# Kernel optimization log

Measured on AMD Instinct MI355X. Metric: run time of the kernel, lower is better.

The kernel has to match this reference:

```python
import jax, jax.numpy as jnp
import numpy as np

B, S, D, H, E = 4, 1024, 1024, 4096, 8


def setup_inputs() -> dict:
    key = jax.random.key(0)
    ks = jax.random.split(key, 5)
    sd = 1.0 / np.sqrt(D)
    sh = 1.0 / np.sqrt(H)
    x = jax.random.normal(ks[0], (B, S, D), dtype=jnp.float32)
    # stacked expert weights: Linear(D->H), ReLU, Linear(H->D)
    W1 = jax.random.normal(ks[1], (E, D, H), dtype=jnp.float32) * sd
    b1 = jnp.zeros((E, H), dtype=jnp.float32)
    W2 = jax.random.normal(ks[2], (E, H, D), dtype=jnp.float32) * sh
    b2 = jnp.zeros((E, D), dtype=jnp.float32)
    # gate Linear(D->E)
    Wg = jax.random.normal(ks[3], (D, E), dtype=jnp.float32) * sd
    bg = jnp.zeros((E,), dtype=jnp.float32)
    return {"x": x, "W1": W1, "b1": b1, "W2": W2, "b2": b2,
            "Wg": Wg, "bg": bg, "top_k": 2}


def reference(x, W1, b1, W2, b2, Wg, bg, top_k):
    # gating
    gating_scores = jnp.einsum('bsd,de->bse', x, Wg) + bg          # [B,S,E]
    gating_probs = jax.nn.softmax(gating_scores, axis=-1)
    _, top_k_indices = jax.lax.top_k(gating_probs, top_k)          # [B,S,K]
    n_exp = Wg.shape[1]
    # per-token 0/1 mask of selected experts (matches torch sum over k of mask)
    # NOTE: original code multiplies by the binary mask only; top_k_probs are
    # computed but NOT used as combine weights. We reproduce that faithfully.
    sel = jnp.sum(top_k_indices[..., None] == jnp.arange(n_exp), axis=2)  # [B,S,E]
    sel = sel.astype(x.dtype)
    # dense all-experts FFN (as the original does)
    h = jax.nn.relu(jnp.einsum('bsd,edh->bseh', x, W1) + b1)       # [B,S,E,H]
    eo = jnp.einsum('bseh,ehd->bsed', h, W2) + b2                  # [B,S,E,D]
    output = jnp.einsum('bsed,bse->bsd', eo, sel)                  # [B,S,D]
    return (output, gating_scores)
```

## Files before the change

kernel.cpp:

```cpp
#include <hip/hip_runtime.h>
#include <hip/hip_bf16.h>
#include <stdint.h>

#define B_ 4
#define S_ 1024
#define D_ 1024
#define H_ 4096
#define E_ 8
#define T_ (B_*S_)

#define BM 256
#define BN 256
#define BK 64

typedef __bf16 bf16x8 __attribute__((ext_vector_type(8)));
typedef float f32x4 __attribute__((ext_vector_type(4)));
typedef unsigned short ushort8 __attribute__((ext_vector_type(8)));

__device__ __forceinline__ unsigned short f2bf(float f) {
  union { float f; uint32_t u; } v; v.f = f;
  uint32_t u = v.u;
  u += 0x7fff + ((u >> 16) & 1);
  return (unsigned short)(u >> 16);
}

__device__ __forceinline__ void gl16(const void* g, void* l) {
  __builtin_amdgcn_global_load_lds(
      (const __attribute__((address_space(1))) void*)g,
      (__attribute__((address_space(3))) void*)l,
      16, 0, 0);
}
#define MEMFENCE asm volatile("" ::: "memory")

__global__ __launch_bounds__(256) void conv_x_kernel(
    const float* __restrict__ x, unsigned short* __restrict__ xb) {
  size_t i = ((size_t)blockIdx.x * 256 + threadIdx.x) * 8;
  const float4* s = (const float4*)(x + i);
  float4 v0 = s[0], v1 = s[1];
  ushort8 w;
  w[0]=f2bf(v0.x); w[1]=f2bf(v0.y); w[2]=f2bf(v0.z); w[3]=f2bf(v0.w);
  w[4]=f2bf(v1.x); w[5]=f2bf(v1.y); w[6]=f2bf(v1.z); w[7]=f2bf(v1.w);
  *(ushort8*)(xb + i) = w;
}

__global__ __launch_bounds__(256) void transpose_conv(
    const float* __restrict__ in, unsigned short* __restrict__ outp,
    int R, int C) {
  __shared__ float tile[64][68];
  const int e = blockIdx.z;
  const size_t eoff = (size_t)e * R * C;
  const int r0 = blockIdx.y * 64, c0 = blockIdx.x * 64;
  const int t = threadIdx.x;
  {
    const int r = t >> 2, cq = (t & 3) * 16;
    const float4* s4 = (const float4*)(in + eoff + (size_t)(r0 + r) * C + (c0 + cq));
#pragma unroll
    for (int i = 0; i < 4; ++i)
      *(float4*)&tile[r][cq + i * 4] = s4[i];
  }
  __syncthreads();
  {
    const int c = t >> 2, r8 = (t & 3) * 16;
    unsigned short* dst = outp + eoff + (size_t)(c0 + c) * R + (r0 + r8);
    ushort8 w0, w1;
#pragma unroll
    for (int j = 0; j < 8; ++j) {
      w0[j] = f2bf(tile[r8 + j][c]);
      w1[j] = f2bf(tile[r8 + 8 + j][c]);
    }
    *(ushort8*)dst = w0;
    *(ushort8*)(dst + 8) = w1;
  }
}

__global__ __launch_bounds__(256) void gating_kernel(
    const float* __restrict__ x, const float* __restrict__ Wg,
    const float* __restrict__ bg, float* __restrict__ scores,
    int* __restrict__ cnt, int* __restrict__ lists) {
  int t = blockIdx.x * 4 + (threadIdx.x >> 6);
  int l = threadIdx.x & 63;
  float acc[E_];
#pragma unroll
  for (int e = 0; e < E_; ++e) acc[e] = 0.f;
  const float* xr = x + (size_t)t * D_;
  for (int k = l; k < D_; k += 64) {
    float xv = xr[k];
    const float4* w = (const float4*)(Wg + (size_t)k * E_);
    float4 w0 = w[0], w1 = w[1];
    acc[0] += xv * w0.x; acc[1] += xv * w0.y; acc[2] += xv * w0.z; acc[3] += xv * w0.w;
    acc[4] += xv * w1.x; acc[5] += xv * w1.y; acc[6] += xv * w1.z; acc[7] += xv * w1.w;
  }
#pragma unroll
  for (int off = 32; off > 0; off >>= 1)
#pragma unroll
    for (int e = 0; e < E_; ++e) acc[e] += __shfl_xor(acc[e], off, 64);
  if (l == 0) {
    float s[E_];
#pragma unroll
    for (int e = 0; e < E_; ++e) {
      s[e] = acc[e] + bg[e];
      scores[(size_t)t * E_ + e] = s[e];
    }
    int i1 = 0; float m1 = -1e30f;
#pragma unroll
    for (int e = 0; e < E_; ++e) if (s[e] > m1) { m1 = s[e]; i1 = e; }
    int i2 = -1; float m2 = -1e30f;
#pragma unroll
    for (int e = 0; e < E_; ++e) if (e != i1 && s[e] > m2) { m2 = s[e]; i2 = e; }
    int p1 = atomicAdd(&cnt[i1], 1); lists[i1 * T_ + p1] = t;
    int p2 = atomicAdd(&cnt[i2], 1); lists[i2 * T_ + p2] = t;
  }
}

__global__ void scan_kernel(const int* __restrict__ cnt, int* __restrict__ off) {
  if (threadIdx.x == 0) {
    int o = 0;
    for (int e = 0; e < E_; ++e) { off[e] = o; o += cnt[e]; }
  }
}

template <int LAYER, int SPLITK>
__global__ __launch_bounds__(512, 2) void ffn_gemm(
    const unsigned short* __restrict__ xb,
    const unsigned short* __restrict__ hbuf,
    const unsigned short* __restrict__ WT,
    const float* __restrict__ bias,
    const int* __restrict__ cnt, const int* __restrict__ off,
    const int* __restrict__ lists,
    unsigned short* __restrict__ hout,
    float* __restrict__ out)
{
  constexpr int K = (LAYER == 1) ? D_ : H_;
  constexpr int N = (LAYER == 1) ? H_ : D_;
  constexpr int KS = K / SPLITK;
  constexpr int NT = KS / BK;

  const int e    = blockIdx.z;
  const int nt_  = blockIdx.x % (N / BN);
  const int sp   = blockIdx.x / (N / BN);
  const int n0   = nt_ * BN;
  const int m0   = blockIdx.y * BM;
  const int k0   = sp * KS;
  const int count = cnt[e];
  if (m0 >= count) return;
  const int oe = off[e];
  const int* lst = lists + e * T_;

  __shared__ unsigned short sA[2][BM * BK];
  __shared__ unsigned short sB[2][BN * BK];

  const int tid  = threadIdx.x;
  const int lane = tid & 63;
  const int wv   = tid >> 6;
  const int wm   = (wv >> 2) * 128;
  const int wn   = (wv & 3) * 64;

  const int srow   = lane >> 3;
  const int schunk = (lane & 7) * 16;
  const int sgoff  = schunk ^ (srow << 4);

  const char* arow[4];
  const char* brow[4];
#pragma unroll
  for (int i = 0; i < 4; ++i) {
    int r  = i * 64 + wv * 8 + srow;
    int gr = m0 + r;
    if (LAYER == 1) {
      int tok = (gr < count) ? lst[gr] : lst[m0];
      arow[i] = (const char*)(xb + (size_t)tok * K + k0);
    } else {
      int rr = (gr < count) ? gr : m0;
      arow[i] = (const char*)(hbuf + (size_t)(oe + rr) * K + k0);
    }
    brow[i] = (const char*)(WT + (size_t)e * N * K + (size_t)(n0 + r) * K + k0);
  }

  auto stage = [&](int buf, int t) {
    const int kb = t * 128;
#pragma unroll
    for (int i = 0; i < 4; ++i)
      gl16(arow[i] + kb + sgoff, (char*)&sA[buf][0] + (i * 64 + wv * 8) * 128);
#pragma unroll
    for (int i = 0; i < 4; ++i)
      gl16(brow[i] + kb + sgoff, (char*)&sB[buf][0] + (i * 64 + wv * 8) * 128);
  };

  const int lrow = lane & 15;
  const int kg   = lane >> 4;
  const int fswz = (lrow & 7) << 4;

  f32x4 acc[8][4];
#pragma unroll
  for (int i = 0; i < 8; ++i)
#pragma unroll
    for (int j = 0; j < 4; ++j) acc[i][j] = (f32x4){0.f, 0.f, 0.f, 0.f};

  stage(0, 0);
  stage(1, 1);
  asm volatile("s_waitcnt vmcnt(8)" ::: "memory");
  __builtin_amdgcn_s_barrier();
  MEMFENCE;

  for (int t = 0; t < NT; ++t) {
    const int buf = t & 1;
    bf16x8 af[8][2], bfm[4][2];
#pragma unroll
    for (int i = 0; i < 8; ++i) {
      const int ra = wm + i * 16 + lrow;
#pragma unroll
      for (int ks = 0; ks < 2; ++ks)
        af[i][ks] = *(const bf16x8*)((const char*)&sA[buf][0] + ra * 128 + ((ks * 64 + kg * 16) ^ fswz));
    }
#pragma unroll
    for (int j = 0; j < 4; ++j) {
      const int rb = wn + j * 16 + lrow;
#pragma unroll
      for (int ks = 0; ks < 2; ++ks)
        bfm[j][ks] = *(const bf16x8*)((const char*)&sB[buf][0] + rb * 128 + ((ks * 64 + kg * 16) ^ fswz));
    }
    MEMFENCE;
    __builtin_amdgcn_s_barrier();
    MEMFENCE;
    if (t + 2 < NT) stage(buf, t + 2);
    __builtin_amdgcn_s_setprio(1);
#pragma unroll
    for (int ks = 0; ks < 2; ++ks)
#pragma unroll
      for (int i = 0; i < 8; ++i)
#pragma unroll
        for (int j = 0; j < 4; ++j)
          acc[i][j] = __builtin_amdgcn_mfma_f32_16x16x32_bf16(af[i][ks], bfm[j][ks], acc[i][j], 0, 0, 0);
    __builtin_amdgcn_s_setprio(0);
    if (t + 2 < NT) {
      asm volatile("s_waitcnt vmcnt(8)" ::: "memory");
    } else if (t + 1 < NT) {
      asm volatile("s_waitcnt vmcnt(0)" ::: "memory");
    }
    MEMFENCE;
    __builtin_amdgcn_s_barrier();
    MEMFENCE;
  }

  const int rbase = 4 * kg;
#pragma unroll
  for (int i = 0; i < 8; ++i) {
#pragma unroll
    for (int r = 0; r < 4; ++r) {
      int row  = wm + i * 16 + rbase + r;
      int grow = m0 + row;
      if (grow < count) {
#pragma unroll
        for (int j = 0; j < 4; ++j) {
          int col  = wn + j * 16 + lrow;
          int gcol = n0 + col;
          float bv = (SPLITK == 1 || sp == 0) ? bias[(size_t)e * N + gcol] : 0.f;
          float v = acc[i][j][r] + bv;
          if (LAYER == 1) {
            v = v > 0.f ? v : 0.f;
            hout[(size_t)(oe + grow) * H_ + gcol] = f2bf(v);
          } else {
            int tok = lst[grow];
            atomicAdd(&out[(size_t)tok * D_ + gcol], v);
          }
        }
      }
    }
  }
}

extern "C" void kernel_launch(void* const* d_in, const int* in_sizes, int n_in,
                              void* d_out, int out_size, void* d_ws, size_t ws_size,
                              hipStream_t stream) {
  (void)in_sizes; (void)n_in; (void)out_size; (void)ws_size;
  const float* x  = (const float*)d_in[0];
  const float* W1 = (const float*)d_in[1];
  const float* b1 = (const float*)d_in[2];
  const float* W2 = (const float*)d_in[3];
  const float* b2 = (const float*)d_in[4];
  const float* Wg = (const float*)d_in[5];
  const float* bg = (const float*)d_in[6];

  float* out    = (float*)d_out;
  float* scores = out + (size_t)T_ * D_;

  char* ws = (char*)d_ws;
  int* cnt   = (int*)ws;
  int* off   = (int*)(ws + 32);
  int* lists = (int*)(ws + 64);
  unsigned short* xb   = (unsigned short*)(ws + 131200);
  unsigned short* hbuf = (unsigned short*)(ws + 131200 + 8388608);
  unsigned short* WT   = (unsigned short*)(ws + 131200 + 8388608 + 67108864);

  hipMemsetAsync(out, 0, (size_t)T_ * D_ * sizeof(float), stream);
  hipMemsetAsync(cnt, 0, 64, stream);

  conv_x_kernel<<<(T_ * D_) / (256 * 8), 256, 0, stream>>>(x, xb);
  gating_kernel<<<T_ / 4, 256, 0, stream>>>(x, Wg, bg, scores, cnt, lists);
  scan_kernel<<<1, 64, 0, stream>>>(cnt, off);

  transpose_conv<<<dim3(H_ / 64, D_ / 64, E_), 256, 0, stream>>>(W1, WT, D_, H_);
  ffn_gemm<1, 1><<<dim3(H_ / BN, T_ / BM, E_), 512, 0, stream>>>(
      xb, hbuf, WT, b1, cnt, off, lists, hbuf, nullptr);

  transpose_conv<<<dim3(D_ / 64, H_ / 64, E_), 256, 0, stream>>>(W2, WT, H_, D_);
  ffn_gemm<2, 2><<<dim3((D_ / BN) * 2, T_ / BM, E_), 512, 0, stream>>>(
      xb, hbuf, WT, b2, cnt, off, lists, nullptr, out);
}
```

Measured before the change: 477.0 us.

## Compact expert tile table and interleave per-phase LDS staging in FFN GEMM

The scan kernel now builds a compact table of (expert, M-tile) pairs, so the GEMM grid only launches blocks for real tiles instead of a dense E x T/BM grid with early exits. The main loop is split into four MFMA phases. Each phase loads a smaller fragment set, and the global-to-LDS loads for the next K-tiles are issued a piece at a time between phases, to spread memory traffic over the compute and cut register pressure. Layer-2 split-K goes from 2 to 4 to add parallelism. The cost is more barriers per K-step and more atomic accumulation traffic into the output.

```diff
diff --git a/kernel.cpp b/kernel.cpp
--- a/kernel.cpp
+++ b/kernel.cpp
@@ -12,6 +12,7 @@
 #define BM 256
 #define BN 256
 #define BK 64
+#define MAXMB 48
 
 typedef __bf16 bf16x8 __attribute__((ext_vector_type(8)));
 typedef float f32x4 __attribute__((ext_vector_type(4)));
@@ -112,10 +113,16 @@
   }
 }
 
-__global__ void scan_kernel(const int* __restrict__ cnt, int* __restrict__ off) {
+__global__ void scan_kernel(const int* __restrict__ cnt, int* __restrict__ off,
+                            int* __restrict__ mbtab) {
   if (threadIdx.x == 0) {
-    int o = 0;
-    for (int e = 0; e < E_; ++e) { off[e] = o; o += cnt[e]; }
+    int o = 0, nb = 0;
+    for (int e = 0; e < E_; ++e) {
+      off[e] = o; o += cnt[e];
+      int ntl = (cnt[e] + BM - 1) / BM;
+      for (int i = 0; i < ntl; ++i) mbtab[nb++] = (e << 16) | i;
+    }
+    for (; nb < MAXMB; ++nb) mbtab[nb] = -1;
   }
 }
 
@@ -126,7 +133,7 @@
     const unsigned short* __restrict__ WT,
     const float* __restrict__ bias,
     const int* __restrict__ cnt, const int* __restrict__ off,
-    const int* __restrict__ lists,
+    const int* __restrict__ lists, const int* __restrict__ mbtab,
     unsigned short* __restrict__ hout,
     float* __restrict__ out)
 {
@@ -134,15 +141,17 @@
   constexpr int N = (LAYER == 1) ? H_ : D_;
   constexpr int KS = K / SPLITK;
   constexpr int NT = KS / BK;
-
-  const int e    = blockIdx.z;
-  const int nt_  = blockIdx.x % (N / BN);
-  const int sp   = blockIdx.x / (N / BN);
-  const int n0   = nt_ * BN;
-  const int m0   = blockIdx.y * BM;
-  const int k0   = sp * KS;
+  constexpr int NX = N / BN;
+
+  const int ent = mbtab[blockIdx.y];
+  if (ent < 0) return;
+  const int e  = ent >> 16;
+  const int m0 = (ent & 0xffff) * BM;
+  const int nt_ = blockIdx.x % NX;
+  const int sp  = blockIdx.x / NX;
+  const int n0  = nt_ * BN;
+  const int k0  = sp * KS;
   const int count = cnt[e];
-  if (m0 >= count) return;
   const int oe = off[e];
   const int* lst = lists + e * T_;
 
@@ -175,19 +184,19 @@
     brow[i] = (const char*)(WT + (size_t)e * N * K + (size_t)(n0 + r) * K + k0);
   }
 
-  auto stage = [&](int buf, int t) {
-    const int kb = t * 128;
-#pragma unroll
-    for (int i = 0; i < 4; ++i)
-      gl16(arow[i] + kb + sgoff, (char*)&sA[buf][0] + (i * 64 + wv * 8) * 128);
-#pragma unroll
-    for (int i = 0; i < 4; ++i)
-      gl16(brow[i] + kb + sgoff, (char*)&sB[buf][0] + (i * 64 + wv * 8) * 128);
+  auto stageA1 = [&](int buf, int t, int ai) {
+    gl16(arow[ai] + t * 128 + sgoff, (char*)&sA[buf][0] + (ai * 64 + wv * 8) * 128);
+  };
+  auto stageB1 = [&](int buf, int t, int bi) {
+    gl16(brow[bi] + t * 128 + sgoff, (char*)&sB[buf][0] + (bi * 64 + wv * 8) * 128);
   };
 
   const int lrow = lane & 15;
   const int kg   = lane >> 4;
   const int fswz = (lrow & 7) << 4;
+  auto frag = [&](const char* base, int row, int ks) {
+    return *(const bf16x8*)(base + row * 128 + ((ks * 64 + kg * 16) ^ fswz));
+  };
 
   f32x4 acc[8][4];
 #pragma unroll
@@ -195,50 +204,90 @@
 #pragma unroll
     for (int j = 0; j < 4; ++j) acc[i][j] = (f32x4){0.f, 0.f, 0.f, 0.f};
 
-  stage(0, 0);
-  stage(1, 1);
-  asm volatile("s_waitcnt vmcnt(8)" ::: "memory");
+#pragma unroll
+  for (int i = 0; i < 4; ++i) stageA1(0, 0, i);
+#pragma unroll
+  for (int i = 0; i < 4; ++i) stageB1(0, 0, i);
+#pragma unroll
+  for (int i = 0; i < 4; ++i) stageB1(1, 1, i);
+  asm volatile("s_waitcnt vmcnt(4)" ::: "memory");
+  MEMFENCE;
   __builtin_amdgcn_s_barrier();
   MEMFENCE;
 
-  for (int t = 0; t < NT; ++t) {
-    const int buf = t & 1;
-    bf16x8 af[8][2], bfm[4][2];
-#pragma unroll
-    for (int i = 0; i < 8; ++i) {
-      const int ra = wm + i * 16 + lrow;
-#pragma unroll
-      for (int ks = 0; ks < 2; ++ks)
-        af[i][ks] = *(const bf16x8*)((const char*)&sA[buf][0] + ra * 128 + ((ks * 64 + kg * 16) ^ fswz));
-    }
-#pragma unroll
-    for (int j = 0; j < 4; ++j) {
-      const int rb = wn + j * 16 + lrow;
-#pragma unroll
-      for (int ks = 0; ks < 2; ++ks)
-        bfm[j][ks] = *(const bf16x8*)((const char*)&sB[buf][0] + rb * 128 + ((ks * 64 + kg * 16) ^ fswz));
-    }
-    MEMFENCE;
-    __builtin_amdgcn_s_barrier();
-    MEMFENCE;
-    if (t + 2 < NT) stage(buf, t + 2);
+  for (int v = 0; v < NT; ++v) {
+    const int buf = v & 1;
+    const char* sAb = (const char*)&sA[buf][0];
+    const char* sBb = (const char*)&sB[buf][0];
+    bf16x8 a0[4], a1[4], b0[4], b1[4];
+
+#pragma unroll
+    for (int i = 0; i < 4; ++i) a0[i] = frag(sAb, wm + i * 16 + lrow, 0);
+#pragma unroll
+    for (int j = 0; j < 4; ++j) b0[j] = frag(sBb, wn + j * 16 + lrow, 0);
+    if (v + 1 < NT) { stageA1(buf ^ 1, v + 1, 0); stageA1(buf ^ 1, v + 1, 2); }
+    MEMFENCE; __builtin_amdgcn_s_barrier();
+    asm volatile("s_waitcnt lgkmcnt(0)" ::: "memory");
+    __builtin_amdgcn_sched_barrier(0);
     __builtin_amdgcn_s_setprio(1);
 #pragma unroll
-    for (int ks = 0; ks < 2; ++ks)
-#pragma unroll
-      for (int i = 0; i < 8; ++i)
-#pragma unroll
-        for (int j = 0; j < 4; ++j)
-          acc[i][j] = __builtin_amdgcn_mfma_f32_16x16x32_bf16(af[i][ks], bfm[j][ks], acc[i][j], 0, 0, 0);
+    for (int i = 0; i < 4; ++i)
+#pragma unroll
+      for (int j = 0; j < 4; ++j)
+        acc[i][j] = __builtin_amdgcn_mfma_f32_16x16x32_bf16(a0[i], b0[j], acc[i][j], 0, 0, 0);
     __builtin_amdgcn_s_setprio(0);
-    if (t + 2 < NT) {
-      asm volatile("s_waitcnt vmcnt(8)" ::: "memory");
-    } else if (t + 1 < NT) {
-      asm volatile("s_waitcnt vmcnt(0)" ::: "memory");
-    }
-    MEMFENCE;
-    __builtin_amdgcn_s_barrier();
-    MEMFENCE;
+    MEMFENCE; __builtin_amdgcn_s_barrier(); MEMFENCE;
+
+#pragma unroll
+    for (int i = 0; i < 4; ++i) a1[i] = frag(sAb, wm + i * 16 + lrow, 1);
+#pragma unroll
+    for (int j = 0; j < 4; ++j) b1[j] = frag(sBb, wn + j * 16 + lrow, 1);
+    if (v + 1 < NT) { stageA1(buf ^ 1, v + 1, 1); stageA1(buf ^ 1, v + 1, 3); }
+    MEMFENCE; __builtin_amdgcn_s_barrier();
+    asm volatile("s_waitcnt lgkmcnt(0)" ::: "memory");
+    __builtin_amdgcn_sched_barrier(0);
+    __builtin_amdgcn_s_setprio(1);
+#pragma unroll
+    for (int i = 0; i < 4; ++i)
+#pragma unroll
+      for (int j = 0; j < 4; ++j)
+        acc[i][j] = __builtin_amdgcn_mfma_f32_16x16x32_bf16(a1[i], b1[j], acc[i][j], 0, 0, 0);
+    __builtin_amdgcn_s_setprio(0);
+    MEMFENCE; __builtin_amdgcn_s_barrier(); MEMFENCE;
+
+#pragma unroll
+    for (int i = 0; i < 4; ++i) a0[i] = frag(sAb, wm + 64 + i * 16 + lrow, 0);
+    if (v + 2 < NT) { stageB1(buf, v + 2, 0); stageB1(buf, v + 2, 1); }
+    MEMFENCE; __builtin_amdgcn_s_barrier();
+    asm volatile("s_waitcnt lgkmcnt(0)" ::: "memory");
+    __builtin_amdgcn_sched_barrier(0);
+    __builtin_amdgcn_s_setprio(1);
+#pragma unroll
+    for (int i = 0; i < 4; ++i)
+#pragma unroll
+      for (int j = 0; j < 4; ++j)
+        acc[4 + i][j] = __builtin_amdgcn_mfma_f32_16x16x32_bf16(a0[i], b0[j], acc[4 + i][j], 0, 0, 0);
+    __builtin_amdgcn_s_setprio(0);
+    MEMFENCE; __builtin_amdgcn_s_barrier(); MEMFENCE;
+
+#pragma unroll
+    for (int i = 0; i < 4; ++i) a1[i] = frag(sAb, wm + 64 + i * 16 + lrow, 1);
+    if (v + 2 < NT) { stageB1(buf, v + 2, 2); stageB1(buf, v + 2, 3); }
+    MEMFENCE; __builtin_amdgcn_s_barrier();
+    asm volatile("s_waitcnt lgkmcnt(0)" ::: "memory");
+    __builtin_amdgcn_sched_barrier(0);
+    __builtin_amdgcn_s_setprio(1);
+#pragma unroll
+    for (int i = 0; i < 4; ++i)
+#pragma unroll
+      for (int j = 0; j < 4; ++j)
+        acc[4 + i][j] = __builtin_amdgcn_mfma_f32_16x16x32_bf16(a1[i], b1[j], acc[4 + i][j], 0, 0, 0);
+    __builtin_amdgcn_s_setprio(0);
+    if (v + 1 < NT) {
+      if (v + 2 < NT) { asm volatile("s_waitcnt vmcnt(4)" ::: "memory"); }
+      else            { asm volatile("s_waitcnt vmcnt(0)" ::: "memory"); }
+    }
+    MEMFENCE; __builtin_amdgcn_s_barrier(); MEMFENCE;
   }
 
   const int rbase = 4 * kg;
@@ -286,23 +335,24 @@
   char* ws = (char*)d_ws;
   int* cnt   = (int*)ws;
   int* off   = (int*)(ws + 32);
-  int* lists = (int*)(ws + 64);
-  unsigned short* xb   = (unsigned short*)(ws + 131200);
-  unsigned short* hbuf = (unsigned short*)(ws + 131200 + 8388608);
-  unsigned short* WT   = (unsigned short*)(ws + 131200 + 8388608 + 67108864);
+  int* mbtab = (int*)(ws + 64);
+  int* lists = (int*)(ws + 256);
+  unsigned short* xb   = (unsigned short*)(ws + 256 + 131072);
+  unsigned short* hbuf = (unsigned short*)(ws + 256 + 131072 + 8388608);
+  unsigned short* WT   = (unsigned short*)(ws + 256 + 131072 + 8388608 + 67108864);
 
   hipMemsetAsync(out, 0, (size_t)T_ * D_ * sizeof(float), stream);
   hipMemsetAsync(cnt, 0, 64, stream);
 
   conv_x_kernel<<<(T_ * D_) / (256 * 8), 256, 0, stream>>>(x, xb);
   gating_kernel<<<T_ / 4, 256, 0, stream>>>(x, Wg, bg, scores, cnt, lists);
-  scan_kernel<<<1, 64, 0, stream>>>(cnt, off);
+  scan_kernel<<<1, 64, 0, stream>>>(cnt, off, mbtab);
 
   transpose_conv<<<dim3(H_ / 64, D_ / 64, E_), 256, 0, stream>>>(W1, WT, D_, H_);
-  ffn_gemm<1, 1><<<dim3(H_ / BN, T_ / BM, E_), 512, 0, stream>>>(
-      xb, hbuf, WT, b1, cnt, off, lists, hbuf, nullptr);
+  ffn_gemm<1, 1><<<dim3(H_ / BN, MAXMB - 8), 512, 0, stream>>>(
+      xb, hbuf, WT, b1, cnt, off, lists, mbtab, hbuf, nullptr);
 
   transpose_conv<<<dim3(D_ / 64, H_ / 64, E_), 256, 0, stream>>>(W2, WT, H_, D_);
-  ffn_gemm<2, 2><<<dim3((D_ / BN) * 2, T_ / BM, E_), 512, 0, stream>>>(
-      xb, hbuf, WT, b2, cnt, off, lists, nullptr, out);
-}
+  ffn_gemm<2, 4><<<dim3((D_ / BN) * 4, MAXMB - 8), 512, 0, stream>>>(
+      xb, hbuf, WT, b2, cnt, off, lists, mbtab, nullptr, out);
+}
```

Result: slower. 540.6 us (+13.3%).

## Schedule expert GEMM tiles via compact task table with XCD-aware block mapping

Applied to the files above, without the earlier changes.

The scan kernel now builds compact task lists of only the valid (expert, m-tile, n-tile, split) tiles for both FFN GEMMs. The GEMMs launch a fixed 1D grid, look up their tile from the table, and remap block IDs so consecutive tasks, which share weight tiles and token rows, land on the same one of 8 XCDs for L2 reuse. This removes the many empty blocks that exited early under the old 3D grid and aims to improve cache locality. It adds a serial single-thread table build and an indirection load per block.

```diff
diff --git a/kernel.cpp b/kernel.cpp
--- a/kernel.cpp
+++ b/kernel.cpp
@@ -12,6 +12,8 @@
 #define BM 256
 #define BN 256
 #define BK 64
+#define MAXT1 640
+#define MAXT2 320
 
 typedef __bf16 bf16x8 __attribute__((ext_vector_type(8)));
 typedef float f32x4 __attribute__((ext_vector_type(4)));
@@ -112,10 +114,29 @@
   }
 }
 
-__global__ void scan_kernel(const int* __restrict__ cnt, int* __restrict__ off) {
+__global__ void scan_kernel(const int* __restrict__ cnt, int* __restrict__ off,
+                            int* __restrict__ hdr, int* __restrict__ t1tab,
+                            int* __restrict__ t2tab) {
   if (threadIdx.x == 0) {
     int o = 0;
-    for (int e = 0; e < E_; ++e) { off[e] = o; o += cnt[e]; }
+    int mtiles[E_];
+    for (int e = 0; e < E_; ++e) {
+      off[e] = o; o += cnt[e];
+      mtiles[e] = (cnt[e] + BM - 1) / BM;
+    }
+    int n1 = 0;
+    for (int e = 0; e < E_; ++e)
+      for (int g = 0; g < 4; ++g)
+        for (int mt = 0; mt < mtiles[e]; ++mt)
+          for (int nl = 0; nl < 4; ++nl)
+            t1tab[n1++] = (e << 20) | (mt << 8) | (g * 4 + nl);
+    int n2 = 0;
+    for (int e = 0; e < E_; ++e)
+      for (int sp = 0; sp < 2; ++sp)
+        for (int mt = 0; mt < mtiles[e]; ++mt)
+          for (int nt = 0; nt < 4; ++nt)
+            t2tab[n2++] = (e << 20) | (mt << 8) | (sp << 4) | nt;
+    hdr[0] = n1; hdr[1] = n2;
   }
 }
 
@@ -127,6 +148,7 @@
     const float* __restrict__ bias,
     const int* __restrict__ cnt, const int* __restrict__ off,
     const int* __restrict__ lists,
+    const int* __restrict__ tab, const int* __restrict__ hdr,
     unsigned short* __restrict__ hout,
     float* __restrict__ out)
 {
@@ -135,14 +157,20 @@
   constexpr int KS = K / SPLITK;
   constexpr int NT = KS / BK;
 
-  const int e    = blockIdx.z;
-  const int nt_  = blockIdx.x % (N / BN);
-  const int sp   = blockIdx.x / (N / BN);
-  const int n0   = nt_ * BN;
-  const int m0   = blockIdx.y * BM;
-  const int k0   = sp * KS;
+  const int ntask = hdr[LAYER - 1];
+  const int b = blockIdx.x;
+  if (b >= ntask) return;
+  const int q = ntask >> 3, r = ntask & 7;
+  const int x = b & 7, ii = b >> 3;
+  const int task = (x < r ? x * (q + 1) : r * (q + 1) + (x - r) * q) + ii;
+
+  const int ent = tab[task];
+  const int e  = ent >> 20;
+  const int m0 = ((ent >> 8) & 0xff) * BM;
+  const int sp = (ent >> 4) & 3;
+  const int n0 = (ent & 15) * BN;
+  const int k0 = sp * KS;
   const int count = cnt[e];
-  if (m0 >= count) return;
   const int oe = off[e];
   const int* lst = lists + e * T_;
 
@@ -163,16 +191,16 @@
   const char* brow[4];
 #pragma unroll
   for (int i = 0; i < 4; ++i) {
-    int r  = i * 64 + wv * 8 + srow;
-    int gr = m0 + r;
+    int rr = i * 64 + wv * 8 + srow;
+    int gr = m0 + rr;
     if (LAYER == 1) {
       int tok = (gr < count) ? lst[gr] : lst[m0];
       arow[i] = (const char*)(xb + (size_t)tok * K + k0);
     } else {
-      int rr = (gr < count) ? gr : m0;
-      arow[i] = (const char*)(hbuf + (size_t)(oe + rr) * K + k0);
-    }
-    brow[i] = (const char*)(WT + (size_t)e * N * K + (size_t)(n0 + r) * K + k0);
+      int r2 = (gr < count) ? gr : m0;
+      arow[i] = (const char*)(hbuf + (size_t)(oe + r2) * K + k0);
+    }
+    brow[i] = (const char*)(WT + (size_t)e * N * K + (size_t)(n0 + rr) * K + k0);
   }
 
   auto stage = [&](int buf, int t) {
@@ -245,8 +273,8 @@
 #pragma unroll
   for (int i = 0; i < 8; ++i) {
 #pragma unroll
-    for (int r = 0; r < 4; ++r) {
-      int row  = wm + i * 16 + rbase + r;
+    for (int r2 = 0; r2 < 4; ++r2) {
+      int row  = wm + i * 16 + rbase + r2;
       int grow = m0 + row;
       if (grow < count) {
 #pragma unroll
@@ -254,7 +282,7 @@
           int col  = wn + j * 16 + lrow;
           int gcol = n0 + col;
           float bv = (SPLITK == 1 || sp == 0) ? bias[(size_t)e * N + gcol] : 0.f;
-          float v = acc[i][j][r] + bv;
+          float v = acc[i][j][r2] + bv;
           if (LAYER == 1) {
             v = v > 0.f ? v : 0.f;
             hout[(size_t)(oe + grow) * H_ + gcol] = f2bf(v);
@@ -286,23 +314,26 @@
   char* ws = (char*)d_ws;
   int* cnt   = (int*)ws;
   int* off   = (int*)(ws + 32);
-  int* lists = (int*)(ws + 64);
-  unsigned short* xb   = (unsigned short*)(ws + 131200);
-  unsigned short* hbuf = (unsigned short*)(ws + 131200 + 8388608);
-  unsigned short* WT   = (unsigned short*)(ws + 131200 + 8388608 + 67108864);
+  int* hdr   = (int*)(ws + 64);
+  int* t1tab = (int*)(ws + 128);
+  int* t2tab = (int*)(ws + 128 + 4 * MAXT1);
+  int* lists = (int*)(ws + 8192);
+  unsigned short* xb   = (unsigned short*)(ws + 8192 + 131072);
+  unsigned short* hbuf = (unsigned short*)(ws + 8192 + 131072 + 8388608);
+  unsigned short* WT   = (unsigned short*)(ws + 8192 + 131072 + 8388608 + 67108864);
 
   hipMemsetAsync(out, 0, (size_t)T_ * D_ * sizeof(float), stream);
   hipMemsetAsync(cnt, 0, 64, stream);
 
   conv_x_kernel<<<(T_ * D_) / (256 * 8), 256, 0, stream>>>(x, xb);
   gating_kernel<<<T_ / 4, 256, 0, stream>>>(x, Wg, bg, scores, cnt, lists);
-  scan_kernel<<<1, 64, 0, stream>>>(cnt, off);
+  scan_kernel<<<1, 64, 0, stream>>>(cnt, off, hdr, t1tab, t2tab);
 
   transpose_conv<<<dim3(H_ / 64, D_ / 64, E_), 256, 0, stream>>>(W1, WT, D_, H_);
-  ffn_gemm<1, 1><<<dim3(H_ / BN, T_ / BM, E_), 512, 0, stream>>>(
-      xb, hbuf, WT, b1, cnt, off, lists, hbuf, nullptr);
+  ffn_gemm<1, 1><<<MAXT1, 512, 0, stream>>>(
+      xb, hbuf, WT, b1, cnt, off, lists, t1tab, hdr, hbuf, nullptr);
 
   transpose_conv<<<dim3(D_ / 64, H_ / 64, E_), 256, 0, stream>>>(W2, WT, H_, D_);
-  ffn_gemm<2, 2><<<dim3((D_ / BN) * 2, T_ / BM, E_), 512, 0, stream>>>(
-      xb, hbuf, WT, b2, cnt, off, lists, nullptr, out);
-}
+  ffn_gemm<2, 2><<<MAXT2, 512, 0, stream>>>(
+      xb, hbuf, WT, b2, cnt, off, lists, t2tab, hdr, nullptr, out);
+}
```

Result: slower. 512.7 us (+7.5%).
